# Optimization experiments

Hardware: AMD Instinct MI355X
Metric: run time of the kernel (lower is better)

## Reference

```python
import jax, jax.numpy as jnp
import numpy as np

N, E, F = 32768, 524288, 16          # nodes, edges, num_filters
S_IN, V_IN = 64, 32                  # input irreps: 64x0e + 32x1o  (dim 64 + 96 = 160)
NRBF = 32                            # radial basis size of f_ij
LN2 = float(np.log(2.0))

def ssp(x):
    # shifted softplus, the standard SchNet activation
    return jax.nn.softplus(x) - LN2

def setup_inputs() -> dict:
    key = jax.random.key(0)
    ks = jax.random.split(key, 16)
    x = jax.random.normal(ks[0], (N, S_IN + 3 * V_IN), jnp.float32)
    idx_i = jax.random.randint(ks[1], (E,), 0, N)
    idx_j = jax.random.randint(ks[2], (E,), 0, N)
    f_ij = jax.random.normal(ks[3], (E, NRBF), jnp.float32)
    rcut_ij = jax.random.uniform(ks[4], (E,), jnp.float32)
    Yr_ij = jax.random.normal(ks[5], (E, 4), jnp.float32)  # 1x0e + 1x1o
    # equivariant Linear 1: (64x0e+32x1o) -> num_filters*(1x0e+1x1o) = 16x0e+16x1o
    W1_0e = jax.random.normal(ks[6], (S_IN, F), jnp.float32)
    W1_1o = jax.random.normal(ks[7], (V_IN, F), jnp.float32)
    # filter MLP: NRBF -> F -> num_irreps(6*F)
    mW1 = jax.random.normal(ks[8], (NRBF, F), jnp.float32) / np.sqrt(NRBF)
    mb1 = jnp.zeros((F,), jnp.float32)
    mW2 = jax.random.normal(ks[9], (F, 6 * F), jnp.float32) / np.sqrt(F)
    mb2 = jnp.zeros((6 * F,), jnp.float32)
    # equivariant Linear 2: (2Fx0e+2Fx1o+Fx1e+Fx2e) -> input irreps (1e/2e paths drop)
    W2_0e = jax.random.normal(ks[10], (2 * F, S_IN), jnp.float32)
    W2_1o = jax.random.normal(ks[11], (2 * F, V_IN), jnp.float32)
    # equivariant Linear 3: input irreps -> input irreps
    W3_0e = jax.random.normal(ks[12], (S_IN, S_IN), jnp.float32)
    W3_1o = jax.random.normal(ks[13], (V_IN, V_IN), jnp.float32)
    return dict(x=x, f_ij=f_ij, rcut_ij=rcut_ij, Yr_ij=Yr_ij,
                W1_0e=W1_0e, W1_1o=W1_1o, mW1=mW1, mb1=mb1, mW2=mW2, mb2=mb2,
                W2_0e=W2_0e, W2_1o=W2_1o, W3_0e=W3_0e, W3_1o=W3_1o,
                idx_i=idx_i, idx_j=idx_j)

def reference(x, f_ij, rcut_ij, Yr_ij, W1_0e, W1_1o, mW1, mb1, mW2, mb2,
              W2_0e, W2_1o, W3_0e, W3_1o, idx_i, idx_j):
    n = x.shape[0]
    s = x[:, :S_IN]                                  # [N, 64]  0e channels
    v = x[:, S_IN:].reshape(n, V_IN, 3)              # [N, 32, 3] 1o channels
    # Linear 1 (per-irrep channel mixing, e3nn fan-in normalization)
    s1 = (s @ W1_0e) / np.sqrt(S_IN)                 # [N, F]
    v1 = jnp.einsum('ncd,cf->nfd', v, W1_1o) / np.sqrt(V_IN)  # [N, F, 3]
    # gather neighbor features (x_j = x[idx_j], mul_to_axis -> per-filter irreps)
    sj = s1[idx_j]                                   # [E, F]
    vj = v1[idx_j]                                   # [E, F, 3]
    y0 = Yr_ij[:, 0]                                 # [E]
    y1 = Yr_ij[:, 1:4]                               # [E, 3]
    # tensor product (0e+1o) x (0e+1o) -> 2x0e + 2x1o + 1x1e + 1x2e, per filter
    o0a = sj * y0[:, None]                                            # 0e: 0e x 0e
    o0b = jnp.einsum('efd,ed->ef', vj, y1) / np.sqrt(3.0)             # 0e: 1o.1o
    o1a = sj[:, :, None] * y1[:, None, :]                             # 1o: 0e x 1o
    o1b = vj * y0[:, None, None]                                      # 1o: 1o x 0e
    o1e = jnp.cross(vj, y1[:, None, :]) / np.sqrt(2.0)                # 1e: 1o ^ 1o
    ux, uy, uz = vj[..., 0], vj[..., 1], vj[..., 2]
    wx, wy, wz = y1[:, None, 0], y1[:, None, 1], y1[:, None, 2]
    o2 = jnp.stack([(ux * wy + uy * wx) / np.sqrt(2.0),
                    (uy * wz + uz * wy) / np.sqrt(2.0),
                    (2.0 * uz * wz - ux * wx - uy * wy) / np.sqrt(6.0),
                    (ux * wz + uz * wx) / np.sqrt(2.0),
                    (ux * wx - uy * wy) / np.sqrt(2.0)], axis=-1)      # 2e [E, F, 5]
    # filter MLP on radial features, gated by cutoff; one scalar per irrep
    W = ssp(f_ij @ mW1 + mb1) @ mW2 + mb2            # [E, 6F]
    W = W * rcut_ij[:, None]
    w0a, w0b, w1a, w1b, w1e, w2 = (W[:, k * F:(k + 1) * F] for k in range(6))
    seg = lambda z: jax.ops.segment_sum(z, idx_i, num_segments=N)
    # modulate + scatter-sum into center atoms
    n0a = seg(o0a * w0a); n0b = seg(o0b * w0b)                          # [N, F]
    n1a = seg(o1a * w1a[:, :, None]); n1b = seg(o1b * w1b[:, :, None])  # [N, F, 3]
    n1e = seg(o1e * w1e[:, :, None])                                    # [N, F, 3] (dropped by Linear 2)
    n2 = seg(o2 * w2[:, :, None])                                       # [N, F, 5] (dropped by Linear 2)
    n0 = jnp.concatenate([n0a, n0b], axis=-1)        # [N, 2F] 0e
    n1 = jnp.concatenate([n1a, n1b], axis=1)         # [N, 2F, 3] 1o
    del n1e, n2  # no matching output irrep in input_irreps -> e3nn Linear drops them
    # Linear 2 back to input irreps
    s2 = (n0 @ W2_0e) / np.sqrt(2 * F)               # [N, 64]
    v2 = jnp.einsum('nfd,fc->ncd', n1, W2_1o) / np.sqrt(2 * F)  # [N, 32, 3]
    # scalar activation on l=0 only
    s2 = ssp(s2)
    # Linear 3
    s3 = (s2 @ W3_0e) / np.sqrt(S_IN)
    v3 = jnp.einsum('ncd,ce->ned', v2, W3_1o) / np.sqrt(V_IN)
    return jnp.concatenate([s3, v3.reshape(n, -1)], axis=-1)  # [N, 160]
```

## Files before the change

kernel.cpp:

```cpp
#include <hip/hip_runtime.h>
#include <math.h>

#define NN 32768
#define NE 524288
#define RSTR 32

__device__ __forceinline__ float sspf(float x) {
    const float INVLN2 = 1.4426950408889634f;
    const float LN2    = 0.69314718055994530942f;
    float t = __builtin_amdgcn_exp2f(-fabsf(x) * INVLN2);
    return fmaxf(x, 0.0f) + LN2 * __builtin_amdgcn_logf(1.0f + t) - LN2;
}

__global__ __launch_bounds__(256) void hist_kernel(
    const int* __restrict__ idx_i, int* __restrict__ counts, int* __restrict__ rank)
{
    int e = blockIdx.x * 256 + threadIdx.x;
    rank[e] = atomicAdd(&counts[idx_i[e]], 1);
}

__global__ __launch_bounds__(1024) void scan_kernel(
    const int* __restrict__ counts, int* __restrict__ start, int* __restrict__ order)
{
    __shared__ int tmp[1024];
    __shared__ int bins[64];
    __shared__ int bcur[64];
    int tid = threadIdx.x;
    int base = tid * 32;
    int cnt[32];
    int local[32];
    int sum = 0;
    const int4* c4 = (const int4*)(counts + base);
#pragma unroll
    for (int q = 0; q < 8; q++) {
        int4 v = c4[q];
        cnt[q*4+0] = v.x; cnt[q*4+1] = v.y; cnt[q*4+2] = v.z; cnt[q*4+3] = v.w;
        local[q*4+0] = sum; sum += v.x;
        local[q*4+1] = sum; sum += v.y;
        local[q*4+2] = sum; sum += v.z;
        local[q*4+3] = sum; sum += v.w;
    }
    tmp[tid] = sum;
    __syncthreads();
    for (int off = 1; off < 1024; off <<= 1) {
        int v = 0;
        if (tid >= off) v = tmp[tid - off];
        __syncthreads();
        if (tid >= off) tmp[tid] += v;
        __syncthreads();
    }
    int excl = tmp[tid] - sum;
#pragma unroll
    for (int k = 0; k < 32; k++) {
        start[base + k] = excl + local[k];
    }
    if (tid == 1023) start[NN] = tmp[1023];

    if (tid < 64) bins[tid] = 0;
    __syncthreads();
#pragma unroll
    for (int k = 0; k < 32; k++) {
        int d = cnt[k] > 63 ? 63 : cnt[k];
        atomicAdd(&bins[63 - d], 1);
    }
    __syncthreads();
    if (tid == 0) {
        int run = 0;
        for (int b = 0; b < 64; b++) { int c = bins[b]; bcur[b] = run; run += c; }
    }
    __syncthreads();
#pragma unroll
    for (int k = 0; k < 32; k++) {
        int d = cnt[k] > 63 ? 63 : cnt[k];
        int pos = atomicAdd(&bcur[63 - d], 1);
        order[pos] = base + k;
    }
}

__global__ __launch_bounds__(256) void eorder_kernel(
    const int* __restrict__ idx_i, const int* __restrict__ start,
    const int* __restrict__ rank, int* __restrict__ eorder)
{
    int e = blockIdx.x * 256 + threadIdx.x;
    eorder[start[idx_i[e]] + rank[e]] = e;
}

__global__ __launch_bounds__(256) void pack_kernel(
    const float* __restrict__ f_ij,
    const float* __restrict__ rcut_ij,
    const float* __restrict__ Yr,
    const int*   __restrict__ idx_j,
    const float* __restrict__ mW1,
    const float* __restrict__ mb1,
    float* __restrict__ epack)
{
    __shared__ float sW1[512];
    __shared__ float sb1[16];
    int t = threadIdx.x;
    for (int k = t; k < 512; k += 256) sW1[k] = mW1[k];
    if (t < 16) sb1[t] = mb1[t];
    __syncthreads();

    int e = blockIdx.x * 256 + t;
    float h[16];
#pragma unroll
    for (int f = 0; f < 16; f++) h[f] = sb1[f];
    const float4* frow = (const float4*)(f_ij + (size_t)e * 32);
#pragma unroll
    for (int rq = 0; rq < 8; rq++) {
        float4 fv = frow[rq];
        int r = rq * 4;
#pragma unroll
        for (int f = 0; f < 16; f++)
            h[f] += fv.x * sW1[(r+0)*16+f] + fv.y * sW1[(r+1)*16+f]
                  + fv.z * sW1[(r+2)*16+f] + fv.w * sW1[(r+3)*16+f];
    }
    float rc = rcut_ij[e];
#pragma unroll
    for (int f = 0; f < 16; f++) h[f] = sspf(h[f]) * rc;

    int j = idx_j[e];
    float4 y = ((const float4*)Yr)[e];

    float* rec = epack + (size_t)e * RSTR;
    float4* r4 = (float4*)rec;
#pragma unroll
    for (int q = 0; q < 4; q++) r4[q] = ((float4*)h)[q];
    r4[4] = y;
    float4 tail; tail.x = rc; tail.y = __int_as_float(j); tail.z = 0.f; tail.w = 0.f;
    r4[5] = tail;
    float4 z; z.x = 0.f; z.y = 0.f; z.z = 0.f; z.w = 0.f;
    r4[6] = z;
    r4[7] = z;
}

__global__ __launch_bounds__(256) void embed_kernel(
    const float* __restrict__ x,
    const float* __restrict__ W1s,
    const float* __restrict__ W1v,
    float* __restrict__ embed)
{
    __shared__ float sWs[1024];
    __shared__ float sWv[512];
    int t = threadIdx.x;
    for (int k = t; k < 1024; k += 256) sWs[k] = W1s[k];
    for (int k = t; k < 512;  k += 256) sWv[k] = W1v[k];
    __syncthreads();

    int n = blockIdx.x * 256 + t;
    const float* xr = x + (size_t)n * 160;

    float s1[16];
#pragma unroll
    for (int f = 0; f < 16; f++) s1[f] = 0.f;
#pragma unroll 1
    for (int cc = 0; cc < 4; cc++) {
        float4 sv[4];
#pragma unroll
        for (int q = 0; q < 4; q++) sv[q] = ((const float4*)xr)[cc*4 + q];
#pragma unroll
        for (int q = 0; q < 4; q++) {
            int c = (cc*4 + q) * 4;
#pragma unroll
            for (int f = 0; f < 16; f++) {
                s1[f] += sv[q].x * sWs[(c+0)*16+f] + sv[q].y * sWs[(c+1)*16+f]
                       + sv[q].z * sWs[(c+2)*16+f] + sv[q].w * sWs[(c+3)*16+f];
            }
        }
    }

    float v1[48];
#pragma unroll
    for (int k = 0; k < 48; k++) v1[k] = 0.f;
#pragma unroll 1
    for (int cc = 0; cc < 4; cc++) {
        float4 vv[6];
#pragma unroll
        for (int q = 0; q < 6; q++) vv[q] = ((const float4*)(xr + 64))[cc*6 + q];
#pragma unroll
        for (int q = 0; q < 6; q++) {
            float vals[4] = {vv[q].x, vv[q].y, vv[q].z, vv[q].w};
#pragma unroll
            for (int u = 0; u < 4; u++) {
                int ml = q * 4 + u;
                int c = cc * 8 + ml / 3;
                int d = ml % 3;
                float val = vals[u];
#pragma unroll
                for (int f = 0; f < 16; f++)
                    v1[f*3+d] += val * sWv[c*16+f];
            }
        }
    }

    float ob[64];
    const float is32 = 0.17677669529663688f;
#pragma unroll
    for (int f = 0; f < 16; f++) {
        ob[f*4+0] = s1[f] * 0.125f;
        ob[f*4+1] = v1[f*3+0] * is32;
        ob[f*4+2] = v1[f*3+1] * is32;
        ob[f*4+3] = v1[f*3+2] * is32;
    }

    float4* eo = (float4*)(embed + (size_t)n * 64);
#pragma unroll
    for (int q = 0; q < 16; q++) eo[q] = ((float4*)ob)[q];
}

__global__ __launch_bounds__(256, 4) void nodeagg_kernel(
    const float* __restrict__ embed,
    const float* __restrict__ epack,
    const int*   __restrict__ start,
    const int*   __restrict__ order,
    const int*   __restrict__ eorder,
    const float* __restrict__ mW2,
    const float* __restrict__ mb2,
    float* __restrict__ acc)
{
    int t = threadIdx.x;
    int gid = blockIdx.x * 256 + t;
    int node = order[gid >> 4];
    int f = gid & 15;

    float wga[16], wgb[16], wgc[16], wgd[16];
#pragma unroll
    for (int k = 0; k < 16; k++) {
        wga[k] = mW2[k*96 + f];
        wgb[k] = mW2[k*96 + 16 + f];
        wgc[k] = mW2[k*96 + 32 + f];
        wgd[k] = mW2[k*96 + 48 + f];
    }
    float b0a = mb2[f], b0b = mb2[16+f], b1a = mb2[32+f], b1b = mb2[48+f];

    float aa = 0.f, ab = 0.f;
    float A1a0 = 0.f, A1a1 = 0.f, A1a2 = 0.f;
    float A1b0 = 0.f, A1b1 = 0.f, A1b2 = 0.f;

    int s0 = start[node];
    int s1 = start[node+1];

    for (int q = s0; q < s1; q++) {
        int e = eorder[q];
        const float4* r4 = (const float4*)(epack + (size_t)e * RSTR);
        float4 h0 = r4[0], h1 = r4[1], h2 = r4[2], h3 = r4[3];
        float4 y  = r4[4], tl = r4[5];
        int j = __float_as_int(tl.y);
        float4 e4 = ((const float4*)(embed + (size_t)j * 64))[f];
        float rc = tl.x;

        float w0a = rc*b0a, w0b = rc*b0b, w1a = rc*b1a, w1b = rc*b1b;
        w0a += h0.x*wga[0]  + h0.y*wga[1]  + h0.z*wga[2]  + h0.w*wga[3]
             + h1.x*wga[4]  + h1.y*wga[5]  + h1.z*wga[6]  + h1.w*wga[7]
             + h2.x*wga[8]  + h2.y*wga[9]  + h2.z*wga[10] + h2.w*wga[11]
             + h3.x*wga[12] + h3.y*wga[13] + h3.z*wga[14] + h3.w*wga[15];
        w0b += h0.x*wgb[0]  + h0.y*wgb[1]  + h0.z*wgb[2]  + h0.w*wgb[3]
             + h1.x*wgb[4]  + h1.y*wgb[5]  + h1.z*wgb[6]  + h1.w*wgb[7]
             + h2.x*wgb[8]  + h2.y*wgb[9]  + h2.z*wgb[10] + h2.w*wgb[11]
             + h3.x*wgb[12] + h3.y*wgb[13] + h3.z*wgb[14] + h3.w*wgb[15];
        w1a += h0.x*wgc[0]  + h0.y*wgc[1]  + h0.z*wgc[2]  + h0.w*wgc[3]
             + h1.x*wgc[4]  + h1.y*wgc[5]  + h1.z*wgc[6]  + h1.w*wgc[7]
             + h2.x*wgc[8]  + h2.y*wgc[9]  + h2.z*wgc[10] + h2.w*wgc[11]
             + h3.x*wgc[12] + h3.y*wgc[13] + h3.z*wgc[14] + h3.w*wgc[15];
        w1b += h0.x*wgd[0]  + h0.y*wgd[1]  + h0.z*wgd[2]  + h0.w*wgd[3]
             + h1.x*wgd[4]  + h1.y*wgd[5]  + h1.z*wgd[6]  + h1.w*wgd[7]
             + h2.x*wgd[8]  + h2.y*wgd[9]  + h2.z*wgd[10] + h2.w*wgd[11]
             + h3.x*wgd[12] + h3.y*wgd[13] + h3.z*wgd[14] + h3.w*wgd[15];

        float sj = e4.x, vx = e4.y, vy = e4.z, vz = e4.w;
        aa += sj * y.x * w0a;
        ab += (vx*y.y + vy*y.z + vz*y.w) * w0b;
        float sw = sj * w1a;
        A1a0 += sw * y.y;
        A1a1 += sw * y.z;
        A1a2 += sw * y.w;
        float yw = y.x * w1b;
        A1b0 += vx * yw;
        A1b1 += vy * yw;
        A1b2 += vz * yw;
    }

    const float is3 = 0.5773502691896258f;
    float* o = acc + (size_t)node * 128;
    o[f]       = aa;
    o[16 + f]  = ab * is3;
    o[32 + f]  = A1a0;
    o[48 + f]  = A1a1;
    o[64 + f]  = A1a2;
    o[80 + f]  = A1b0;
    o[96 + f]  = A1b1;
    o[112 + f] = A1b2;
}


template<int LEN>
__device__ __forceinline__ void v2_seg(const float* a, int d, int cb,
    const float* __restrict__ W2v, float* V2, int ln)
{
    cb = __builtin_amdgcn_readfirstlane(cb);
    d  = __builtin_amdgcn_readfirstlane(d);
    const float is32 = 0.17677669529663688f;
    float na[16], nb[16];
    const float4* pa = (const float4*)(a + 32 + 16*d);
    const float4* pb = (const float4*)(a + 80 + 16*d);
#pragma unroll
    for (int q = 0; q < 4; q++) { ((float4*)na)[q] = pa[q]; ((float4*)nb)[q] = pb[q]; }
    float tacc[LEN];
#pragma unroll
    for (int c = 0; c < LEN; c++) tacc[c] = 0.f;
#pragma unroll
    for (int f = 0; f < 16; f++) {
        float fa = na[f], fb = nb[f];
#pragma unroll
        for (int c = 0; c < LEN; c++)
            tacc[c] += fa * W2v[f*32 + cb + c] + fb * W2v[(16+f)*32 + cb + c];
    }
    float* row = V2 + (d*64 + ln) * 33 + cb;
#pragma unroll
    for (int c = 0; c < LEN; c++) row[c] = tacc[c] * is32;
}

template<int LEN>
__device__ __forceinline__ void v3_seg(float* o, int d, int cb,
    const float* __restrict__ W3v, const float* V2, int ln)
{
    cb = __builtin_amdgcn_readfirstlane(cb);
    d  = __builtin_amdgcn_readfirstlane(d);
    const float is32 = 0.17677669529663688f;
    float tacc[LEN];
#pragma unroll
    for (int c = 0; c < LEN; c++) tacc[c] = 0.f;
    const float* row = V2 + (d*64 + ln) * 33;
#pragma unroll
    for (int k = 0; k < 32; k++) {
        float vk = row[k];
#pragma unroll
        for (int c = 0; c < LEN; c++) tacc[c] += vk * W3v[k*32 + cb + c];
    }
#pragma unroll
    for (int c = 0; c < LEN; c++) o[64 + (cb+c)*3 + d] = tacc[c] * is32;
}

__global__ __launch_bounds__(512, 4) void out_kernel(
    const float* __restrict__ acc,
    const float* __restrict__ W2s,
    const float* __restrict__ W2v,
    const float* __restrict__ W3s,
    const float* __restrict__ W3v,
    float* __restrict__ out)
{
    __shared__ float S2[64*65];
    __shared__ float V2[3*64*33];
    int t = threadIdx.x;
    int w = t >> 6, ln = t & 63;
    int node = blockIdx.x * 64 + ln;
    const float* a = acc + (size_t)node * 128;
    float* o = out + (size_t)node * 160;
    const float is32 = 0.17677669529663688f;

    if (w < 4) {
        int cb = __builtin_amdgcn_readfirstlane(w * 16);
        float n0r[32];
#pragma unroll
        for (int q = 0; q < 8; q++) ((float4*)n0r)[q] = ((const float4*)a)[q];
        float tacc[16];
#pragma unroll
        for (int c = 0; c < 16; c++) tacc[c] = 0.f;
#pragma unroll
        for (int k = 0; k < 32; k++) {
            float nk = n0r[k];
#pragma unroll
            for (int c = 0; c < 16; c++) tacc[c] += nk * W2s[k*64 + cb + c];
        }
        float* row = S2 + ln*65 + cb;
#pragma unroll
        for (int c = 0; c < 16; c++) row[c] = sspf(tacc[c] * is32);
    } else if (w == 4) {
        v2_seg<24>(a, 0, 0,  W2v, V2, ln);
    } else if (w == 5) {
        v2_seg<8> (a, 0, 24, W2v, V2, ln);
        v2_seg<16>(a, 1, 0,  W2v, V2, ln);
    } else if (w == 6) {
        v2_seg<16>(a, 1, 16, W2v, V2, ln);
        v2_seg<8> (a, 2, 0,  W2v, V2, ln);
    } else {
        v2_seg<24>(a, 2, 8,  W2v, V2, ln);
    }
    __syncthreads();
    if (w < 4) {
        int cb = __builtin_amdgcn_readfirstlane(w * 16);
        float tacc[16];
#pragma unroll
        for (int c = 0; c < 16; c++) tacc[c] = 0.f;
        const float* row = S2 + ln*65;
#pragma unroll
        for (int k = 0; k < 64; k++) {
            float sk = row[k];
#pragma unroll
            for (int c = 0; c < 16; c++) tacc[c] += sk * W3s[k*64 + cb + c];
        }
#pragma unroll
        for (int q = 0; q < 4; q++) {
            float4 r = {tacc[q*4+0]*0.125f, tacc[q*4+1]*0.125f,
                        tacc[q*4+2]*0.125f, tacc[q*4+3]*0.125f};
            ((float4*)(o + cb))[q] = r;
        }
    } else if (w == 4) {
        v3_seg<24>(o, 0, 0,  W3v, V2, ln);
    } else if (w == 5) {
        v3_seg<8> (o, 0, 24, W3v, V2, ln);
        v3_seg<16>(o, 1, 0,  W3v, V2, ln);
    } else if (w == 6) {
        v3_seg<16>(o, 1, 16, W3v, V2, ln);
        v3_seg<8> (o, 2, 0,  W3v, V2, ln);
    } else {
        v3_seg<24>(o, 2, 8,  W3v, V2, ln);
    }
}

extern "C" void kernel_launch(void* const* d_in, const int* in_sizes, int n_in,
                              void* d_out, int out_size, void* d_ws, size_t ws_size,
                              hipStream_t stream) {
    const float* x     = (const float*)d_in[0];
    const float* f_ij  = (const float*)d_in[1];
    const float* rcut  = (const float*)d_in[2];
    const float* Yr    = (const float*)d_in[3];
    const float* W1s   = (const float*)d_in[4];
    const float* W1v   = (const float*)d_in[5];
    const float* mW1   = (const float*)d_in[6];
    const float* mb1   = (const float*)d_in[7];
    const float* mW2   = (const float*)d_in[8];
    const float* mb2   = (const float*)d_in[9];
    const float* W2s   = (const float*)d_in[10];
    const float* W2v   = (const float*)d_in[11];
    const float* W3s   = (const float*)d_in[12];
    const float* W3v   = (const float*)d_in[13];
    const int*   idx_i = (const int*)d_in[14];
    const int*   idx_j = (const int*)d_in[15];
    float* out = (float*)d_out;

    float* fws   = (float*)d_ws;
    float* embed = fws;
    float* acc   = embed + (size_t)NN * 64;
    float* epack = acc   + (size_t)NN * 128;
    int* ibase   = (int*)(epack + (size_t)NE * RSTR);
    int* counts  = ibase;
    int* start   = counts + NN;
    int* rank    = start + NN + 1;
    int* order   = rank + NE;
    int* eorder  = order + NN;

    hipMemsetAsync(counts, 0, (size_t)NN * sizeof(int), stream);
    hist_kernel<<<NE/256, 256, 0, stream>>>(idx_i, counts, rank);
    scan_kernel<<<1, 1024, 0, stream>>>(counts, start, order);
    eorder_kernel<<<NE/256, 256, 0, stream>>>(idx_i, start, rank, eorder);
    pack_kernel<<<NE/256, 256, 0, stream>>>(f_ij, rcut, Yr, idx_j,
                                            mW1, mb1, epack);
    embed_kernel<<<NN/256, 256, 0, stream>>>(x, W1s, W1v, embed);
    nodeagg_kernel<<<(NN*16)/256, 256, 0, stream>>>(embed, epack, start, order,
                                                    eorder, mW2, mb2, acc);
    out_kernel<<<NN/64, 512, 0, stream>>>(acc, W2s, W2v, W3s, W3v, out);
}
```

Measured before the change: 353.4 us.

## Fuse radial filter MLP first layer into node aggregation kernel via lane shuffles

Removes the pack kernel that computed the first filter-MLP layer per edge and wrote a 128-byte packed edge record, and instead computes it inside the node aggregation loop. Each of the 16 lanes in a node group loads two f_ij values, the group exchanges them with cross-lane shuffles to compute one hidden unit per lane, and a second shuffle loop broadcasts the hidden vector for the mW2 products. This removes a full write and re-read of the packed edge buffer. In exchange it adds many shuffles and LDS weight reads per edge iteration, and reads f_ij, Yr, rcut and idx_j as separate scattered gathers.

```diff
diff --git a/kernel.cpp b/kernel.cpp
--- a/kernel.cpp
+++ b/kernel.cpp
@@ -3,7 +3,6 @@
 
 #define NN 32768
 #define NE 524288
-#define RSTR 32
 
 __device__ __forceinline__ float sspf(float x) {
     const float INVLN2 = 1.4426950408889634f;
@@ -85,14 +84,94 @@
     eorder[start[idx_i[e]] + rank[e]] = e;
 }
 
-__global__ __launch_bounds__(256) void pack_kernel(
+__global__ __launch_bounds__(256) void embed_kernel(
+    const float* __restrict__ x,
+    const float* __restrict__ W1s,
+    const float* __restrict__ W1v,
+    float* __restrict__ embed)
+{
+    __shared__ float sWs[1024];
+    __shared__ float sWv[512];
+    int t = threadIdx.x;
+    for (int k = t; k < 1024; k += 256) sWs[k] = W1s[k];
+    for (int k = t; k < 512;  k += 256) sWv[k] = W1v[k];
+    __syncthreads();
+
+    int n = blockIdx.x * 256 + t;
+    const float* xr = x + (size_t)n * 160;
+
+    float s1[16];
+#pragma unroll
+    for (int f = 0; f < 16; f++) s1[f] = 0.f;
+#pragma unroll 1
+    for (int cc = 0; cc < 4; cc++) {
+        float4 sv[4];
+#pragma unroll
+        for (int q = 0; q < 4; q++) sv[q] = ((const float4*)xr)[cc*4 + q];
+#pragma unroll
+        for (int q = 0; q < 4; q++) {
+            int c = (cc*4 + q) * 4;
+#pragma unroll
+            for (int f = 0; f < 16; f++) {
+                s1[f] += sv[q].x * sWs[(c+0)*16+f] + sv[q].y * sWs[(c+1)*16+f]
+                       + sv[q].z * sWs[(c+2)*16+f] + sv[q].w * sWs[(c+3)*16+f];
+            }
+        }
+    }
+
+    float v1[48];
+#pragma unroll
+    for (int k = 0; k < 48; k++) v1[k] = 0.f;
+#pragma unroll 1
+    for (int cc = 0; cc < 4; cc++) {
+        float4 vv[6];
+#pragma unroll
+        for (int q = 0; q < 6; q++) vv[q] = ((const float4*)(xr + 64))[cc*6 + q];
+#pragma unroll
+        for (int q = 0; q < 6; q++) {
+            float vals[4] = {vv[q].x, vv[q].y, vv[q].z, vv[q].w};
+#pragma unroll
+            for (int u = 0; u < 4; u++) {
+                int ml = q * 4 + u;
+                int c = cc * 8 + ml / 3;
+                int d = ml % 3;
+                float val = vals[u];
+#pragma unroll
+                for (int f = 0; f < 16; f++)
+                    v1[f*3+d] += val * sWv[c*16+f];
+            }
+        }
+    }
+
+    float ob[64];
+    const float is32 = 0.17677669529663688f;
+#pragma unroll
+    for (int f = 0; f < 16; f++) {
+        ob[f*4+0] = s1[f] * 0.125f;
+        ob[f*4+1] = v1[f*3+0] * is32;
+        ob[f*4+2] = v1[f*3+1] * is32;
+        ob[f*4+3] = v1[f*3+2] * is32;
+    }
+
+    float4* eo = (float4*)(embed + (size_t)n * 64);
+#pragma unroll
+    for (int q = 0; q < 16; q++) eo[q] = ((float4*)ob)[q];
+}
+
+__global__ __launch_bounds__(256, 4) void nodeagg_kernel(
+    const float* __restrict__ embed,
     const float* __restrict__ f_ij,
     const float* __restrict__ rcut_ij,
     const float* __restrict__ Yr,
     const int*   __restrict__ idx_j,
+    const int*   __restrict__ start,
+    const int*   __restrict__ order,
+    const int*   __restrict__ eorder,
     const float* __restrict__ mW1,
     const float* __restrict__ mb1,
-    float* __restrict__ epack)
+    const float* __restrict__ mW2,
+    const float* __restrict__ mb2,
+    float* __restrict__ acc)
 {
     __shared__ float sW1[512];
     __shared__ float sb1[16];
@@ -101,127 +180,11 @@
     if (t < 16) sb1[t] = mb1[t];
     __syncthreads();
 
-    int e = blockIdx.x * 256 + t;
-    float h[16];
-#pragma unroll
-    for (int f = 0; f < 16; f++) h[f] = sb1[f];
-    const float4* frow = (const float4*)(f_ij + (size_t)e * 32);
-#pragma unroll
-    for (int rq = 0; rq < 8; rq++) {
-        float4 fv = frow[rq];
-        int r = rq * 4;
-#pragma unroll
-        for (int f = 0; f < 16; f++)
-            h[f] += fv.x * sW1[(r+0)*16+f] + fv.y * sW1[(r+1)*16+f]
-                  + fv.z * sW1[(r+2)*16+f] + fv.w * sW1[(r+3)*16+f];
-    }
-    float rc = rcut_ij[e];
-#pragma unroll
-    for (int f = 0; f < 16; f++) h[f] = sspf(h[f]) * rc;
-
-    int j = idx_j[e];
-    float4 y = ((const float4*)Yr)[e];
-
-    float* rec = epack + (size_t)e * RSTR;
-    float4* r4 = (float4*)rec;
-#pragma unroll
-    for (int q = 0; q < 4; q++) r4[q] = ((float4*)h)[q];
-    r4[4] = y;
-    float4 tail; tail.x = rc; tail.y = __int_as_float(j); tail.z = 0.f; tail.w = 0.f;
-    r4[5] = tail;
-    float4 z; z.x = 0.f; z.y = 0.f; z.z = 0.f; z.w = 0.f;
-    r4[6] = z;
-    r4[7] = z;
-}
-
-__global__ __launch_bounds__(256) void embed_kernel(
-    const float* __restrict__ x,
-    const float* __restrict__ W1s,
-    const float* __restrict__ W1v,
-    float* __restrict__ embed)
-{
-    __shared__ float sWs[1024];
-    __shared__ float sWv[512];
-    int t = threadIdx.x;
-    for (int k = t; k < 1024; k += 256) sWs[k] = W1s[k];
-    for (int k = t; k < 512;  k += 256) sWv[k] = W1v[k];
-    __syncthreads();
-
-    int n = blockIdx.x * 256 + t;
-    const float* xr = x + (size_t)n * 160;
-
-    float s1[16];
-#pragma unroll
-    for (int f = 0; f < 16; f++) s1[f] = 0.f;
-#pragma unroll 1
-    for (int cc = 0; cc < 4; cc++) {
-        float4 sv[4];
-#pragma unroll
-        for (int q = 0; q < 4; q++) sv[q] = ((const float4*)xr)[cc*4 + q];
-#pragma unroll
-        for (int q = 0; q < 4; q++) {
-            int c = (cc*4 + q) * 4;
-#pragma unroll
-            for (int f = 0; f < 16; f++) {
-                s1[f] += sv[q].x * sWs[(c+0)*16+f] + sv[q].y * sWs[(c+1)*16+f]
-                       + sv[q].z * sWs[(c+2)*16+f] + sv[q].w * sWs[(c+3)*16+f];
-            }
-        }
-    }
-
-    float v1[48];
-#pragma unroll
-    for (int k = 0; k < 48; k++) v1[k] = 0.f;
-#pragma unroll 1
-    for (int cc = 0; cc < 4; cc++) {
-        float4 vv[6];
-#pragma unroll
-        for (int q = 0; q < 6; q++) vv[q] = ((const float4*)(xr + 64))[cc*6 + q];
-#pragma unroll
-        for (int q = 0; q < 6; q++) {
-            float vals[4] = {vv[q].x, vv[q].y, vv[q].z, vv[q].w};
-#pragma unroll
-            for (int u = 0; u < 4; u++) {
-                int ml = q * 4 + u;
-                int c = cc * 8 + ml / 3;
-                int d = ml % 3;
-                float val = vals[u];
-#pragma unroll
-                for (int f = 0; f < 16; f++)
-                    v1[f*3+d] += val * sWv[c*16+f];
-            }
-        }
-    }
-
-    float ob[64];
-    const float is32 = 0.17677669529663688f;
-#pragma unroll
-    for (int f = 0; f < 16; f++) {
-        ob[f*4+0] = s1[f] * 0.125f;
-        ob[f*4+1] = v1[f*3+0] * is32;
-        ob[f*4+2] = v1[f*3+1] * is32;
-        ob[f*4+3] = v1[f*3+2] * is32;
-    }
-
-    float4* eo = (float4*)(embed + (size_t)n * 64);
-#pragma unroll
-    for (int q = 0; q < 16; q++) eo[q] = ((float4*)ob)[q];
-}
-
-__global__ __launch_bounds__(256, 4) void nodeagg_kernel(
-    const float* __restrict__ embed,
-    const float* __restrict__ epack,
-    const int*   __restrict__ start,
-    const int*   __restrict__ order,
-    const int*   __restrict__ eorder,
-    const float* __restrict__ mW2,
-    const float* __restrict__ mb2,
-    float* __restrict__ acc)
-{
-    int t = threadIdx.x;
     int gid = blockIdx.x * 256 + t;
     int node = order[gid >> 4];
     int f = gid & 15;
+    int lane = t & 63;
+    int gb = lane & 48;
 
     float wga[16], wgb[16], wgc[16], wgd[16];
 #pragma unroll
@@ -232,6 +195,7 @@
         wgd[k] = mW2[k*96 + 48 + f];
     }
     float b0a = mb2[f], b0b = mb2[16+f], b1a = mb2[32+f], b1b = mb2[48+f];
+    float b1f = sb1[f];
 
     float aa = 0.f, ab = 0.f;
     float A1a0 = 0.f, A1a1 = 0.f, A1a2 = 0.f;
@@ -242,30 +206,30 @@
 
     for (int q = s0; q < s1; q++) {
         int e = eorder[q];
-        const float4* r4 = (const float4*)(epack + (size_t)e * RSTR);
-        float4 h0 = r4[0], h1 = r4[1], h2 = r4[2], h3 = r4[3];
-        float4 y  = r4[4], tl = r4[5];
-        int j = __float_as_int(tl.y);
+        float2 fv = *(const float2*)(f_ij + (size_t)e * 32 + 2*f);
+        float4 y  = ((const float4*)Yr)[e];
+        float rc  = rcut_ij[e];
+        int j     = idx_j[e];
         float4 e4 = ((const float4*)(embed + (size_t)j * 64))[f];
-        float rc = tl.x;
+
+        float hf = b1f;
+#pragma unroll
+        for (int k = 0; k < 16; k++) {
+            float a0 = __shfl(fv.x, gb + k, 64);
+            float a1 = __shfl(fv.y, gb + k, 64);
+            hf += a0 * sW1[(2*k)*16 + f] + a1 * sW1[(2*k+1)*16 + f];
+        }
+        hf = sspf(hf) * rc;
 
         float w0a = rc*b0a, w0b = rc*b0b, w1a = rc*b1a, w1b = rc*b1b;
-        w0a += h0.x*wga[0]  + h0.y*wga[1]  + h0.z*wga[2]  + h0.w*wga[3]
-             + h1.x*wga[4]  + h1.y*wga[5]  + h1.z*wga[6]  + h1.w*wga[7]
-             + h2.x*wga[8]  + h2.y*wga[9]  + h2.z*wga[10] + h2.w*wga[11]
-             + h3.x*wga[12] + h3.y*wga[13] + h3.z*wga[14] + h3.w*wga[15];
-        w0b += h0.x*wgb[0]  + h0.y*wgb[1]  + h0.z*wgb[2]  + h0.w*wgb[3]
-             + h1.x*wgb[4]  + h1.y*wgb[5]  + h1.z*wgb[6]  + h1.w*wgb[7]
-             + h2.x*wgb[8]  + h2.y*wgb[9]  + h2.z*wgb[10] + h2.w*wgb[11]
-             + h3.x*wgb[12] + h3.y*wgb[13] + h3.z*wgb[14] + h3.w*wgb[15];
-        w1a += h0.x*wgc[0]  + h0.y*wgc[1]  + h0.z*wgc[2]  + h0.w*wgc[3]
-             + h1.x*wgc[4]  + h1.y*wgc[5]  + h1.z*wgc[6]  + h1.w*wgc[7]
-             + h2.x*wgc[8]  + h2.y*wgc[9]  + h2.z*wgc[10] + h2.w*wgc[11]
-             + h3.x*wgc[12] + h3.y*wgc[13] + h3.z*wgc[14] + h3.w*wgc[15];
-        w1b += h0.x*wgd[0]  + h0.y*wgd[1]  + h0.z*wgd[2]  + h0.w*wgd[3]
-             + h1.x*wgd[4]  + h1.y*wgd[5]  + h1.z*wgd[6]  + h1.w*wgd[7]
-             + h2.x*wgd[8]  + h2.y*wgd[9]  + h2.z*wgd[10] + h2.w*wgd[11]
-             + h3.x*wgd[12] + h3.y*wgd[13] + h3.z*wgd[14] + h3.w*wgd[15];
+#pragma unroll
+        for (int k = 0; k < 16; k++) {
+            float hk = __shfl(hf, gb + k, 64);
+            w0a += hk * wga[k];
+            w0b += hk * wgb[k];
+            w1a += hk * wgc[k];
+            w1b += hk * wgd[k];
+        }
 
         float sj = e4.x, vx = e4.y, vy = e4.z, vz = e4.w;
         aa += sj * y.x * w0a;
@@ -442,8 +406,7 @@
     float* fws   = (float*)d_ws;
     float* embed = fws;
     float* acc   = embed + (size_t)NN * 64;
-    float* epack = acc   + (size_t)NN * 128;
-    int* ibase   = (int*)(epack + (size_t)NE * RSTR);
+    int* ibase   = (int*)(acc + (size_t)NN * 128);
     int* counts  = ibase;
     int* start   = counts + NN;
     int* rank    = start + NN + 1;
@@ -454,10 +417,9 @@
     hist_kernel<<<NE/256, 256, 0, stream>>>(idx_i, counts, rank);
     scan_kernel<<<1, 1024, 0, stream>>>(counts, start, order);
     eorder_kernel<<<NE/256, 256, 0, stream>>>(idx_i, start, rank, eorder);
-    pack_kernel<<<NE/256, 256, 0, stream>>>(f_ij, rcut, Yr, idx_j,
-                                            mW1, mb1, epack);
     embed_kernel<<<NN/256, 256, 0, stream>>>(x, W1s, W1v, embed);
-    nodeagg_kernel<<<(NN*16)/256, 256, 0, stream>>>(embed, epack, start, order,
-                                                    eorder, mW2, mb2, acc);
+    nodeagg_kernel<<<(NN*16)/256, 256, 0, stream>>>(embed, f_ij, rcut, Yr, idx_j,
+                                                    start, order, eorder,
+                                                    mW1, mb1, mW2, mb2, acc);
     out_kernel<<<NN/64, 512, 0, stream>>>(acc, W2s, W2v, W3s, W3v, out);
 }
```

Measured after the change: 559.8 us. 58.4% more time.
